# Performance work log

Hardware: AMD Instinct MI355X
Metric: run time of the kernel (lower is better)

Reference implementation:

```python
import jax, jax.numpy as jnp
import numpy as np

NEG_SLOPE = 0.2  # PyG GATConv default negative_slope


def _gat_conv(x, edge_index, W, att_src, att_dst, bias, heads, out_ch, concat):
    """PyG-style GATConv with add_self_loops=False, shared src/dst lin.
    x: [N, F_in], edge_index: [2, E] (row 0 = src j, row 1 = dst i).
    W: [F_in, heads*out_ch]; att_src/att_dst: [heads, out_ch]; bias: [heads*out_ch] or [out_ch].
    """
    N = x.shape[0]
    src, dst = edge_index[0], edge_index[1]
    h = (x @ W).reshape(N, heads, out_ch)                      # [N, H, C]
    a_src = jnp.einsum('nhc,hc->nh', h, att_src)               # [N, H]
    a_dst = jnp.einsum('nhc,hc->nh', h, att_dst)               # [N, H]
    e = a_src[src] + a_dst[dst]                                # [E, H]
    e = jnp.where(e > 0, e, NEG_SLOPE * e)                     # leaky_relu
    # segment softmax over edges sharing the same destination
    m = jax.ops.segment_max(e, dst, num_segments=N)            # [N, H]
    e = jnp.exp(e - m[dst])                                    # [E, H]
    s = jax.ops.segment_sum(e, dst, num_segments=N)            # [N, H]
    alpha = e / (s[dst] + 1e-16)                               # [E, H]
    msg = h[src] * alpha[:, :, None]                           # [E, H, C]
    out = jax.ops.segment_sum(msg, dst, num_segments=N)        # [N, H, C]
    if concat:
        out = out.reshape(N, heads * out_ch)
    else:
        out = out.mean(axis=1)
    return out + bias


def setup_inputs() -> dict:
    key = jax.random.key(0)
    ks = jax.random.split(key, 12)
    N, E = 100000, 1600000
    dinp, dhid, dout, heads = 128, 32, 128, 4
    x = jax.random.normal(ks[0], (N, dinp), dtype=jnp.float32)
    a = jax.random.randint(ks[1], (2, E), 0, N, dtype=jnp.int64)
    s1 = 1.0 / np.sqrt(dinp)
    s2 = 1.0 / np.sqrt(dhid * heads)
    return {
        'x': x,
        'a': a,
        'W1': jax.random.normal(ks[2], (dinp, heads * dhid), dtype=jnp.float32) * s1,
        'att_src1': jax.random.normal(ks[3], (heads, dhid), dtype=jnp.float32) * s1,
        'att_dst1': jax.random.normal(ks[4], (heads, dhid), dtype=jnp.float32) * s1,
        'b1': jnp.zeros((heads * dhid,), dtype=jnp.float32),
        'W2': jax.random.normal(ks[5], (heads * dhid, dout), dtype=jnp.float32) * s2,
        'att_src2': jax.random.normal(ks[6], (1, dout), dtype=jnp.float32) * s2,
        'att_dst2': jax.random.normal(ks[7], (1, dout), dtype=jnp.float32) * s2,
        'b2': jnp.zeros((dout,), dtype=jnp.float32),
    }


def reference(x, a, W1, att_src1, att_dst1, b1, W2, att_src2, att_dst2, b2):
    heads, dhid, dout = 4, 32, 128
    h = _gat_conv(x, a, W1, att_src1, att_dst1, b1, heads, dhid, concat=True)
    h = jax.nn.elu(h)
    out = _gat_conv(h, a, W2, att_src2, att_dst2, b2, 1, dout, concat=False)
    return jax.nn.elu(out)
```

## Files before the change

kernel.cpp:

```cpp
#include <hip/hip_runtime.h>
#include <hip/hip_fp16.h>
#include <math.h>


typedef _Float16 f16x8 __attribute__((ext_vector_type(8)));
typedef float    f32x4 __attribute__((ext_vector_type(4)));


__global__ __launch_bounds__(256) void k_hist(const int* __restrict__ dst,
                                              int* __restrict__ bcnt, int E, int NBUCK) {
    __shared__ int lh[1024];
    int t = threadIdx.x;
    for (int i = t; i < NBUCK; i += 256) lh[i] = 0;
    __syncthreads();
    for (int e = blockIdx.x * 256 + t; e < E; e += gridDim.x * 256)
        atomicAdd(&lh[dst[e] >> 7], 1);
    __syncthreads();
    for (int i = t; i < NBUCK; i += 256) {
        int c = lh[i];
        if (c) atomicAdd(&bcnt[i], c);
    }
}

__global__ void k_bscan(const int* __restrict__ bcnt, int* __restrict__ bbase,
                        int* __restrict__ bcur, int* __restrict__ off,
                        int NBUCK, int N, int E) {
    __shared__ int sd[1024];
    int t = threadIdx.x;
    int v = (t < NBUCK) ? bcnt[t] : 0;
    sd[t] = v; __syncthreads();
    for (int ofs = 1; ofs < 1024; ofs <<= 1) {
        int w = (t >= ofs) ? sd[t - ofs] : 0;
        __syncthreads();
        sd[t] += w;
        __syncthreads();
    }
    if (t < NBUCK) { int ex = sd[t] - v; bbase[t] = ex; bcur[t] = ex; }
    if (t == 0) { bbase[NBUCK] = E; off[N] = E; }
}

__global__ __launch_bounds__(256) void k_binscatter(
    const int* __restrict__ src, const int* __restrict__ dst,
    int* __restrict__ bcur, int* __restrict__ tmp, int E, int NBUCK) {
    __shared__ int lh[1024], lbase[1024];
    int t = threadIdx.x;
    for (int i = t; i < NBUCK; i += 256) lh[i] = 0;
    __syncthreads();
    int tbeg = blockIdx.x * 8192;
    int tend = tbeg + 8192; if (tend > E) tend = E;
    for (int e = tbeg + t; e < tend; e += 256) atomicAdd(&lh[dst[e] >> 7], 1);
    __syncthreads();
    for (int i = t; i < NBUCK; i += 256) {
        int c = lh[i];
        lbase[i] = c ? atomicAdd(&bcur[i], c) : 0;
        lh[i] = 0;
    }
    __syncthreads();
    for (int e = tbeg + t; e < tend; e += 256) {
        int d = dst[e];
        int b = d >> 7;
        int r = atomicAdd(&lh[b], 1);
        tmp[lbase[b] + r] = (src[e] << 7) | (d & 127);
    }
}

__global__ __launch_bounds__(256) void k_bsort(
    const int* __restrict__ tmp, const int* __restrict__ bbase,
    int* __restrict__ off, int* __restrict__ esrc, int N) {
    __shared__ int h[128], hs[128], cur[128];
    int b = blockIdx.x, t = threadIdx.x;
    int base = bbase[b];
    int cnt  = bbase[b + 1] - base;
    int node0 = b << 7;
    if (t < 128) h[t] = 0;
    __syncthreads();
    for (int i = t; i < cnt; i += 256) atomicAdd(&h[tmp[base + i] & 127], 1);
    __syncthreads();
    if (t < 128) hs[t] = h[t];
    __syncthreads();
    for (int ofs = 1; ofs < 128; ofs <<= 1) {
        int w = (t < 128 && t >= ofs) ? hs[t - ofs] : 0;
        __syncthreads();
        if (t < 128) hs[t] += w;
        __syncthreads();
    }
    if (t < 128) {
        int ex = hs[t] - h[t];
        if (node0 + t < N) off[node0 + t] = base + ex;
        cur[t] = base + ex;
    }
    __syncthreads();
    for (int i = t; i < cnt; i += 256) {
        int p = tmp[base + i];
        int pos = atomicAdd(&cur[p & 127], 1);
        esrc[pos] = p >> 7;
    }
}


template <int H, typename TI>
__global__ __launch_bounds__(256, 3) void k_gemm_mfma(
    const TI* __restrict__ X, const float* __restrict__ Wg,
    const float* __restrict__ att_s, const float* __restrict__ att_d,
    __half* __restrict__ Y, float* __restrict__ as_, float* __restrict__ ad_, int N)
{
    __shared__ _Float16 Wf[8][4][512];
    __shared__ _Float16 Xh[64][136];
    const int t = threadIdx.x;
    const int lane = t & 63;
    const int wv = t >> 6;
    const int m = lane & 15;
    const int q = lane >> 4;

    for (int f = t; f < 2048; f += 256) {
        int nt = f >> 8, ks = (f >> 6) & 3, ls = f & 63;
        int qq = ls >> 4, mm = ls & 15;
        int col = nt * 16 + mm;
        int k0  = ks * 32 + qq * 8;
        f16x8 frag;
#pragma unroll
        for (int j = 0; j < 8; j++)
            frag[j] = (_Float16)Wg[(size_t)(k0 + j) * 128 + col];
        *(f16x8*)&Wf[nt][ks][ls * 8] = frag;
    }

    float atts_v[8], attd_v[8];
#pragma unroll
    for (int nt = 0; nt < 8; nt++) {
        atts_v[nt] = att_s[nt * 16 + m];
        attd_v[nt] = att_d[nt * 16 + m];
    }
    __syncthreads();

    for (int base = blockIdx.x * 64; base < N; base += gridDim.x * 64) {
        for (int i = t; i < 1024; i += 256) {
            int r = i >> 4, c8 = i & 15;
            int gr = base + r;
            _Float16* d = &Xh[r][c8 * 8];
            if (gr < N) {
                if constexpr (sizeof(TI) == 4) {
                    const float4* s = (const float4*)((const float*)X + (size_t)gr * 128 + c8 * 8);
                    float4 x0 = s[0], x1 = s[1];
                    d[0] = (_Float16)x0.x; d[1] = (_Float16)x0.y;
                    d[2] = (_Float16)x0.z; d[3] = (_Float16)x0.w;
                    d[4] = (_Float16)x1.x; d[5] = (_Float16)x1.y;
                    d[6] = (_Float16)x1.z; d[7] = (_Float16)x1.w;
                } else {
                    *(uint4*)d = *(const uint4*)((const __half*)X + (size_t)gr * 128 + c8 * 8);
                }
            } else {
                uint4 z; z.x = 0; z.y = 0; z.z = 0; z.w = 0;
                *(uint4*)d = z;
            }
        }
        __syncthreads();

        const int rowb = base + wv * 16;

        f16x8 af[4];
#pragma unroll
        for (int ks = 0; ks < 4; ks++)
            af[ks] = *(const f16x8*)&Xh[wv * 16 + m][ks * 32 + q * 8];

        f32x4 acc[8];
#pragma unroll
        for (int nt = 0; nt < 8; nt++) { acc[nt][0] = 0.f; acc[nt][1] = 0.f; acc[nt][2] = 0.f; acc[nt][3] = 0.f; }

#pragma unroll
        for (int nt = 0; nt < 8; nt++) {
            f16x8 b0v = *(const f16x8*)&Wf[nt][0][lane * 8];
            f16x8 b1v = *(const f16x8*)&Wf[nt][1][lane * 8];
            f16x8 b2v = *(const f16x8*)&Wf[nt][2][lane * 8];
            f16x8 b3v = *(const f16x8*)&Wf[nt][3][lane * 8];
            acc[nt] = __builtin_amdgcn_mfma_f32_16x16x32_f16(af[0], b0v, acc[nt], 0, 0, 0);
            acc[nt] = __builtin_amdgcn_mfma_f32_16x16x32_f16(af[1], b1v, acc[nt], 0, 0, 0);
            acc[nt] = __builtin_amdgcn_mfma_f32_16x16x32_f16(af[2], b2v, acc[nt], 0, 0, 0);
            acc[nt] = __builtin_amdgcn_mfma_f32_16x16x32_f16(af[3], b3v, acc[nt], 0, 0, 0);
        }

#pragma unroll
        for (int nt = 0; nt < 8; nt++) {
#pragma unroll
            for (int i = 0; i < 4; i++) {
                int r = rowb + q * 4 + i;
                if (r < N) Y[(size_t)r * 128 + nt * 16 + m] = __float2half(acc[nt][i]);
            }
        }

        if (H == 4) {
            float ph[4][4], pdv[4][4];
#pragma unroll
            for (int h = 0; h < 4; h++)
#pragma unroll
                for (int i = 0; i < 4; i++) {
                    ph[h][i]  = acc[2 * h][i] * atts_v[2 * h] + acc[2 * h + 1][i] * atts_v[2 * h + 1];
                    pdv[h][i] = acc[2 * h][i] * attd_v[2 * h] + acc[2 * h + 1][i] * attd_v[2 * h + 1];
                }
#pragma unroll
            for (int lvl = 0; lvl < 4; lvl++) {
                const int msk = 1 << lvl;
#pragma unroll
                for (int h = 0; h < 4; h++)
#pragma unroll
                    for (int i = 0; i < 4; i++) {
                        ph[h][i]  += __shfl_xor(ph[h][i], msk, 64);
                        pdv[h][i] += __shfl_xor(pdv[h][i], msk, 64);
                    }
            }
            if (m == 0) {
#pragma unroll
                for (int i = 0; i < 4; i++) {
                    int r = rowb + q * 4 + i;
                    if (r < N) {
#pragma unroll
                        for (int h = 0; h < 4; h++) {
                            as_[(size_t)r * 4 + h] = ph[h][i];
                            ad_[(size_t)r * 4 + h] = pdv[h][i];
                        }
                    }
                }
            }
        } else {
            float ps[4], pdv[4];
#pragma unroll
            for (int i = 0; i < 4; i++) {
                float s = 0.f, dsum = 0.f;
#pragma unroll
                for (int nt = 0; nt < 8; nt++) {
                    s    += acc[nt][i] * atts_v[nt];
                    dsum += acc[nt][i] * attd_v[nt];
                }
                ps[i] = s; pdv[i] = dsum;
            }
#pragma unroll
            for (int lvl = 0; lvl < 4; lvl++) {
                const int msk = 1 << lvl;
#pragma unroll
                for (int i = 0; i < 4; i++) {
                    ps[i]  += __shfl_xor(ps[i], msk, 64);
                    pdv[i] += __shfl_xor(pdv[i], msk, 64);
                }
            }
            if (m == 0) {
#pragma unroll
                for (int i = 0; i < 4; i++) {
                    int r = rowb + q * 4 + i;
                    if (r < N) { as_[r] = ps[i]; ad_[r] = pdv[i]; }
                }
            }
        }
        __syncthreads();
    }
}


template <int H, typename TO>
__global__ __launch_bounds__(256) void k_agg(
    const __half* __restrict__ feat,
    const float* __restrict__ asrc,
    const float* __restrict__ adst,
    const int*   __restrict__ off,
    const int*   __restrict__ esrc,
    const float* __restrict__ bias,
    TO*          __restrict__ out,
    int N)
{
    __shared__ __attribute__((aligned(16))) int   sj[4][64];
    __shared__ __attribute__((aligned(16))) float sp[4][64 * H];

    int wave = threadIdx.x >> 6;
    int lane = threadIdx.x & 63;
    int node = (blockIdx.x * 256 + threadIdx.x) >> 6;
    if (node >= N) return;
    int beg = off[node], end = off[node + 1];

    float adst_i[H];
#pragma unroll
    for (int h = 0; h < H; h++) adst_i[h] = adst[(size_t)node * H + h];

    const int g    = lane >> 4;
    const int sub  = lane & 15;
    const int head = (H == 4) ? (sub >> 2) : 0;
    const __half* fb = feat + sub * 8;

    float o0 = 0.f, o1 = 0.f, o2 = 0.f, o3 = 0.f;
    float o4 = 0.f, o5 = 0.f, o6 = 0.f, o7 = 0.f;
    float ssum = 0.f;

    auto accum8 = [&](const __half* hp, float aa) {
        ssum += aa;
        o0 = fmaf(aa, __half2float(hp[0]), o0);
        o1 = fmaf(aa, __half2float(hp[1]), o1);
        o2 = fmaf(aa, __half2float(hp[2]), o2);
        o3 = fmaf(aa, __half2float(hp[3]), o3);
        o4 = fmaf(aa, __half2float(hp[4]), o4);
        o5 = fmaf(aa, __half2float(hp[5]), o5);
        o6 = fmaf(aa, __half2float(hp[6]), o6);
        o7 = fmaf(aa, __half2float(hp[7]), o7);
    };

    for (int cbeg = beg; cbeg < end; cbeg += 64) {
        int cnt = end - cbeg; if (cnt > 64) cnt = 64;
        if (lane < cnt) {
            int j = esrc[cbeg + lane];
            sj[wave][lane] = j;
            if (H == 4) {
                float4 av = *(const float4*)(asrc + (size_t)j * 4);
                float e;
                e = av.x + adst_i[0]; e = e > 0.f ? e : 0.2f * e; sp[wave][0 * 64 + lane] = __expf(e);
                e = av.y + adst_i[1]; e = e > 0.f ? e : 0.2f * e; sp[wave][1 * 64 + lane] = __expf(e);
                e = av.z + adst_i[2]; e = e > 0.f ? e : 0.2f * e; sp[wave][2 * 64 + lane] = __expf(e);
                e = av.w + adst_i[3]; e = e > 0.f ? e : 0.2f * e; sp[wave][3 * 64 + lane] = __expf(e);
            } else {
                float e = asrc[j] + adst_i[0];
                e = e > 0.f ? e : 0.2f * e;
                sp[wave][lane] = __expf(e);
            }
        }
        asm volatile("s_waitcnt lgkmcnt(0)" ::: "memory");

        for (int b0 = 0; b0 < cnt; b0 += 16) {
            float aa[4]; uint4 hv[4];
#pragma unroll
            for (int u = 0; u < 4; u++) {
                int e  = b0 + 4 * u + g;
                bool ok = e < cnt;
                int ec = ok ? e : 0;
                int j  = sj[wave][ec];
                aa[u]  = ok ? sp[wave][head * 64 + ec] : 0.f;
                hv[u]  = *(const uint4*)(fb + (size_t)j * 128);
            }
            accum8((const __half*)&hv[0], aa[0]);
            accum8((const __half*)&hv[1], aa[1]);
            accum8((const __half*)&hv[2], aa[2]);
            accum8((const __half*)&hv[3], aa[3]);
        }
    }

    o0 += __shfl_xor(o0, 16, 64); o0 += __shfl_xor(o0, 32, 64);
    o1 += __shfl_xor(o1, 16, 64); o1 += __shfl_xor(o1, 32, 64);
    o2 += __shfl_xor(o2, 16, 64); o2 += __shfl_xor(o2, 32, 64);
    o3 += __shfl_xor(o3, 16, 64); o3 += __shfl_xor(o3, 32, 64);
    o4 += __shfl_xor(o4, 16, 64); o4 += __shfl_xor(o4, 32, 64);
    o5 += __shfl_xor(o5, 16, 64); o5 += __shfl_xor(o5, 32, 64);
    o6 += __shfl_xor(o6, 16, 64); o6 += __shfl_xor(o6, 32, 64);
    o7 += __shfl_xor(o7, 16, 64); o7 += __shfl_xor(o7, 32, 64);
    ssum += __shfl_xor(ssum, 16, 64);
    ssum += __shfl_xor(ssum, 32, 64);

    float so0 = o0, so1 = o1;
    so0 = (g == 1) ? o2 : so0;  so1 = (g == 1) ? o3 : so1;
    so0 = (g == 2) ? o4 : so0;  so1 = (g == 2) ? o5 : so1;
    so0 = (g == 3) ? o6 : so0;  so1 = (g == 3) ? o7 : so1;

    const int c2 = sub * 8 + 2 * g;
    float inv = 1.f / (ssum + 1e-16f);
    float r0 = so0 * inv + bias[c2];
    float r1 = so1 * inv + bias[c2 + 1];
    float e0 = __expf(r0) - 1.0f;
    float e1 = __expf(r1) - 1.0f;
    r0 = r0 > 0.f ? r0 : e0;
    r1 = r1 > 0.f ? r1 : e1;

    if constexpr (sizeof(TO) == 2) {
        *(__half2*)((__half*)out + (size_t)node * 128 + c2) = __floats2half2_rn(r0, r1);
    } else {
        *(float2*)((float*)out + (size_t)node * 128 + c2) = make_float2(r0, r1);
    }
}


extern "C" void kernel_launch(void* const* d_in, const int* in_sizes, int n_in,
                              void* d_out, int out_size, void* d_ws, size_t ws_size,
                              hipStream_t stream)
{
    const float* x    = (const float*)d_in[0];
    const int*   a    = (const int*)  d_in[1];
    const float* W1   = (const float*)d_in[2];
    const float* as1w = (const float*)d_in[3];
    const float* ad1w = (const float*)d_in[4];
    const float* b1   = (const float*)d_in[5];
    const float* W2   = (const float*)d_in[6];
    const float* as2w = (const float*)d_in[7];
    const float* ad2w = (const float*)d_in[8];
    const float* b2   = (const float*)d_in[9];

    const int N = in_sizes[0] / 128;
    const int E = in_sizes[1] / 2;
    const int* srcA = a;
    const int* dstA = a + E;
    const int NBUCK = (N + 127) >> 7;

    char* ws = (char*)d_ws;
    size_t o = 0;
    auto alloc = [&](size_t bytes) -> void* {
        void* p = ws + o;
        o += (bytes + 255) & ~(size_t)255;
        return p;
    };
    __half* hbuf  = (__half*)alloc((size_t)N * 128 * 2);
    __half* hact  = (__half*)alloc((size_t)N * 128 * 2);
    float*  as1   = (float*) alloc((size_t)N * 4 * 4);
    float*  ad1   = (float*) alloc((size_t)N * 4 * 4);
    float*  as2   = (float*) alloc((size_t)N * 4);
    float*  ad2   = (float*) alloc((size_t)N * 4);
    int*    off   = (int*)   alloc((size_t)(N + 1) * 4);
    int*    esrc  = (int*)   alloc((size_t)E * 4);
    int*    tmp   = (int*)   alloc((size_t)E * 4);
    int*    bcnt  = (int*)   alloc(1024 * 4);
    int*    bbase = (int*)   alloc(1025 * 4);
    int*    bcur  = (int*)   alloc(1024 * 4);

    hipMemsetAsync(bcnt, 0, (size_t)NBUCK * 4, stream);
    k_hist<<<256, 256, 0, stream>>>(dstA, bcnt, E, NBUCK);
    k_bscan<<<1, 1024, 0, stream>>>(bcnt, bbase, bcur, off, NBUCK, N, E);
    k_binscatter<<<(E + 8191) / 8192, 256, 0, stream>>>(srcA, dstA, bcur, tmp, E, NBUCK);
    k_bsort<<<NBUCK, 256, 0, stream>>>(tmp, bbase, off, esrc, N);

    k_gemm_mfma<4, float><<<768, 256, 0, stream>>>(x, W1, as1w, ad1w, hbuf, as1, ad1, N);
    k_agg<4, __half><<<(N + 3) / 4, 256, 0, stream>>>(hbuf, as1, ad1, off, esrc, b1, hact, N);

    k_gemm_mfma<1, __half><<<768, 256, 0, stream>>>(hact, W2, as2w, ad2w, hbuf, as2, ad2, N);
    k_agg<1, float><<<(N + 3) / 4, 256, 0, stream>>>(hbuf, as2, ad2, off, esrc, b2, (float*)d_out, N);
}
```

Baseline: 340.6 us.

## Fuse layer-1 aggregation with layer-2 GEMM and attention logits

New measurement: 350.3 us. 2.9% more time.

```diff
diff --git a/kernel.cpp b/kernel.cpp
--- a/kernel.cpp
+++ b/kernel.cpp
@@ -24,9 +24,18 @@
 
 __global__ void k_bscan(const int* __restrict__ bcnt, int* __restrict__ bbase,
                         int* __restrict__ bcur, int* __restrict__ off,
-                        int NBUCK, int N, int E) {
+                        int NBUCK, int N, int E,
+                        const float* __restrict__ W2g, _Float16* __restrict__ W2f) {
     __shared__ int sd[1024];
     int t = threadIdx.x;
+    for (int f = t; f < 2048; f += 1024) {
+        int nt = f >> 8, ks = (f >> 6) & 3, ls = f & 63;
+        int col = nt * 16 + (ls & 15);
+        int k0  = ks * 32 + (ls >> 4) * 8;
+#pragma unroll
+        for (int j = 0; j < 8; j++)
+            W2f[(size_t)f * 8 + j] = (_Float16)W2g[(size_t)(k0 + j) * 128 + col];
+    }
     int v = (t < NBUCK) ? bcnt[t] : 0;
     sd[t] = v; __syncthreads();
     for (int ofs = 1; ofs < 1024; ofs <<= 1) {
@@ -254,6 +263,188 @@
 }
 
 
+__global__ __launch_bounds__(256) void k_agg_g2(
+    const __half* __restrict__ feat,
+    const float* __restrict__ asrc,
+    const float* __restrict__ adst,
+    const int*   __restrict__ off,
+    const int*   __restrict__ esrc,
+    const float* __restrict__ bias,
+    const _Float16* __restrict__ W2f,
+    const float* __restrict__ att_s2,
+    const float* __restrict__ att_d2,
+    __half* __restrict__ Y2,
+    float* __restrict__ as2, float* __restrict__ ad2, int N)
+{
+    __shared__ __attribute__((aligned(16))) int      sj[4][64];
+    __shared__ __attribute__((aligned(16))) float    sp[4][256];
+    __shared__ __attribute__((aligned(16))) _Float16 rows[16][136];
+    __shared__ float sps[4][16], spd[4][16];
+
+    const int wave = threadIdx.x >> 6;
+    const int lane = threadIdx.x & 63;
+    const int g    = lane >> 4;
+    const int sub  = lane & 15;
+    const int head = sub >> 2;
+    const __half* fb = feat + sub * 8;
+    const int nodeBase = blockIdx.x * 16;
+
+    for (int it = 0; it < 4; it++) {
+        const int node = nodeBase + wave * 4 + it;
+        int beg = 0, end = 0;
+        float ad0 = 0.f, ad1v = 0.f, ad2v = 0.f, ad3v = 0.f;
+        if (node < N) {
+            beg = off[node]; end = off[node + 1];
+            const float* ap = adst + (size_t)node * 4;
+            ad0 = ap[0]; ad1v = ap[1]; ad2v = ap[2]; ad3v = ap[3];
+        }
+
+        float o0 = 0.f, o1 = 0.f, o2 = 0.f, o3 = 0.f;
+        float o4 = 0.f, o5 = 0.f, o6 = 0.f, o7 = 0.f;
+        float ssum = 0.f;
+
+        auto accum8 = [&](const __half* hp, float aa) {
+            ssum += aa;
+            o0 = fmaf(aa, __half2float(hp[0]), o0);
+            o1 = fmaf(aa, __half2float(hp[1]), o1);
+            o2 = fmaf(aa, __half2float(hp[2]), o2);
+            o3 = fmaf(aa, __half2float(hp[3]), o3);
+            o4 = fmaf(aa, __half2float(hp[4]), o4);
+            o5 = fmaf(aa, __half2float(hp[5]), o5);
+            o6 = fmaf(aa, __half2float(hp[6]), o6);
+            o7 = fmaf(aa, __half2float(hp[7]), o7);
+        };
+
+        for (int cbeg = beg; cbeg < end; cbeg += 64) {
+            int cnt = end - cbeg; if (cnt > 64) cnt = 64;
+            if (lane < cnt) {
+                int j = esrc[cbeg + lane];
+                sj[wave][lane] = j;
+                float4 av = *(const float4*)(asrc + (size_t)j * 4);
+                float e;
+                e = av.x + ad0;  e = e > 0.f ? e : 0.2f * e; sp[wave][0 * 64 + lane] = __expf(e);
+                e = av.y + ad1v; e = e > 0.f ? e : 0.2f * e; sp[wave][1 * 64 + lane] = __expf(e);
+                e = av.z + ad2v; e = e > 0.f ? e : 0.2f * e; sp[wave][2 * 64 + lane] = __expf(e);
+                e = av.w + ad3v; e = e > 0.f ? e : 0.2f * e; sp[wave][3 * 64 + lane] = __expf(e);
+            }
+            asm volatile("s_waitcnt lgkmcnt(0)" ::: "memory");
+
+            for (int b0 = 0; b0 < cnt; b0 += 16) {
+                float aa[4]; uint4 hv[4];
+#pragma unroll
+                for (int u = 0; u < 4; u++) {
+                    int e  = b0 + 4 * u + g;
+                    bool ok = e < cnt;
+                    int ec = ok ? e : 0;
+                    int j  = sj[wave][ec];
+                    aa[u]  = ok ? sp[wave][head * 64 + ec] : 0.f;
+                    hv[u]  = *(const uint4*)(fb + (size_t)j * 128);
+                }
+                accum8((const __half*)&hv[0], aa[0]);
+                accum8((const __half*)&hv[1], aa[1]);
+                accum8((const __half*)&hv[2], aa[2]);
+                accum8((const __half*)&hv[3], aa[3]);
+            }
+        }
+
+        o0 += __shfl_xor(o0, 16, 64); o0 += __shfl_xor(o0, 32, 64);
+        o1 += __shfl_xor(o1, 16, 64); o1 += __shfl_xor(o1, 32, 64);
+        o2 += __shfl_xor(o2, 16, 64); o2 += __shfl_xor(o2, 32, 64);
+        o3 += __shfl_xor(o3, 16, 64); o3 += __shfl_xor(o3, 32, 64);
+        o4 += __shfl_xor(o4, 16, 64); o4 += __shfl_xor(o4, 32, 64);
+        o5 += __shfl_xor(o5, 16, 64); o5 += __shfl_xor(o5, 32, 64);
+        o6 += __shfl_xor(o6, 16, 64); o6 += __shfl_xor(o6, 32, 64);
+        o7 += __shfl_xor(o7, 16, 64); o7 += __shfl_xor(o7, 32, 64);
+        ssum += __shfl_xor(ssum, 16, 64);
+        ssum += __shfl_xor(ssum, 32, 64);
+
+        float so0 = o0, so1 = o1;
+        so0 = (g == 1) ? o2 : so0;  so1 = (g == 1) ? o3 : so1;
+        so0 = (g == 2) ? o4 : so0;  so1 = (g == 2) ? o5 : so1;
+        so0 = (g == 3) ? o6 : so0;  so1 = (g == 3) ? o7 : so1;
+
+        const int c2 = sub * 8 + 2 * g;
+        float inv = 1.f / (ssum + 1e-16f);
+        float r0 = so0 * inv + bias[c2];
+        float r1 = so1 * inv + bias[c2 + 1];
+        float e0 = __expf(r0) - 1.0f;
+        float e1 = __expf(r1) - 1.0f;
+        r0 = r0 > 0.f ? r0 : e0;
+        r1 = r1 > 0.f ? r1 : e1;
+
+        _Float16* rp = &rows[wave * 4 + it][c2];
+        rp[0] = (_Float16)r0;
+        rp[1] = (_Float16)r1;
+    }
+    __syncthreads();
+
+    const int m = lane & 15;
+    const int q = lane >> 4;
+
+    f16x8 af[4];
+#pragma unroll
+    for (int ks = 0; ks < 4; ks++)
+        af[ks] = *(const f16x8*)&rows[m][ks * 32 + q * 8];
+
+    f32x4 acc[2];
+    float a2s[2], a2d[2];
+#pragma unroll
+    for (int u = 0; u < 2; u++) {
+        const int nt = wave * 2 + u;
+        a2s[u] = att_s2[nt * 16 + m];
+        a2d[u] = att_d2[nt * 16 + m];
+        acc[u][0] = 0.f; acc[u][1] = 0.f; acc[u][2] = 0.f; acc[u][3] = 0.f;
+#pragma unroll
+        for (int ks = 0; ks < 4; ks++) {
+            f16x8 bv = *(const f16x8*)(W2f + ((size_t)(nt * 4 + ks) * 512 + lane * 8));
+            acc[u] = __builtin_amdgcn_mfma_f32_16x16x32_f16(af[ks], bv, acc[u], 0, 0, 0);
+        }
+    }
+
+#pragma unroll
+    for (int u = 0; u < 2; u++) {
+        const int col = (wave * 2 + u) * 16 + m;
+#pragma unroll
+        for (int i = 0; i < 4; i++) {
+            int r = nodeBase + q * 4 + i;
+            if (r < N) Y2[(size_t)r * 128 + col] = __float2half(acc[u][i]);
+        }
+    }
+
+    float ps[4], pd[4];
+#pragma unroll
+    for (int i = 0; i < 4; i++) {
+        ps[i] = acc[0][i] * a2s[0] + acc[1][i] * a2s[1];
+        pd[i] = acc[0][i] * a2d[0] + acc[1][i] * a2d[1];
+    }
+#pragma unroll
+    for (int lvl = 0; lvl < 4; lvl++) {
+        const int msk = 1 << lvl;
+#pragma unroll
+        for (int i = 0; i < 4; i++) {
+            ps[i] += __shfl_xor(ps[i], msk, 64);
+            pd[i] += __shfl_xor(pd[i], msk, 64);
+        }
+    }
+    if (m == 0) {
+#pragma unroll
+        for (int i = 0; i < 4; i++) {
+            sps[wave][q * 4 + i] = ps[i];
+            spd[wave][q * 4 + i] = pd[i];
+        }
+    }
+    __syncthreads();
+
+    if (wave == 0 && lane < 16) {
+        int node = nodeBase + lane;
+        if (node < N) {
+            as2[node] = sps[0][lane] + sps[1][lane] + sps[2][lane] + sps[3][lane];
+            ad2[node] = spd[0][lane] + spd[1][lane] + spd[2][lane] + spd[3][lane];
+        }
+    }
+}
+
+
 template <int H, typename TO>
 __global__ __launch_bounds__(256) void k_agg(
     const __half* __restrict__ feat,
@@ -398,28 +589,30 @@
         o += (bytes + 255) & ~(size_t)255;
         return p;
     };
-    __half* hbuf  = (__half*)alloc((size_t)N * 128 * 2);
-    __half* hact  = (__half*)alloc((size_t)N * 128 * 2);
-    float*  as1   = (float*) alloc((size_t)N * 4 * 4);
-    float*  ad1   = (float*) alloc((size_t)N * 4 * 4);
-    float*  as2   = (float*) alloc((size_t)N * 4);
-    float*  ad2   = (float*) alloc((size_t)N * 4);
-    int*    off   = (int*)   alloc((size_t)(N + 1) * 4);
-    int*    esrc  = (int*)   alloc((size_t)E * 4);
-    int*    tmp   = (int*)   alloc((size_t)E * 4);
-    int*    bcnt  = (int*)   alloc(1024 * 4);
-    int*    bbase = (int*)   alloc(1025 * 4);
-    int*    bcur  = (int*)   alloc(1024 * 4);
+    __half*    hbuf = (__half*)   alloc((size_t)N * 128 * 2);
+    __half*    y2   = (__half*)   alloc((size_t)N * 128 * 2);
+    float*     as1  = (float*)    alloc((size_t)N * 4 * 4);
+    float*     ad1  = (float*)    alloc((size_t)N * 4 * 4);
+    float*     as2  = (float*)    alloc((size_t)N * 4);
+    float*     ad2  = (float*)    alloc((size_t)N * 4);
+    int*       off  = (int*)      alloc((size_t)(N + 1) * 4);
+    int*       esrc = (int*)      alloc((size_t)E * 4);
+    int*       tmp  = (int*)      alloc((size_t)E * 4);
+    int*       bcnt = (int*)      alloc(1024 * 4);
+    int*       bbase= (int*)      alloc(1025 * 4);
+    int*       bcur = (int*)      alloc(1024 * 4);
+    _Float16*  w2f  = (_Float16*) alloc((size_t)2048 * 16);
 
     hipMemsetAsync(bcnt, 0, (size_t)NBUCK * 4, stream);
     k_hist<<<256, 256, 0, stream>>>(dstA, bcnt, E, NBUCK);
-    k_bscan<<<1, 1024, 0, stream>>>(bcnt, bbase, bcur, off, NBUCK, N, E);
+    k_bscan<<<1, 1024, 0, stream>>>(bcnt, bbase, bcur, off, NBUCK, N, E, W2, w2f);
     k_binscatter<<<(E + 8191) / 8192, 256, 0, stream>>>(srcA, dstA, bcur, tmp, E, NBUCK);
     k_bsort<<<NBUCK, 256, 0, stream>>>(tmp, bbase, off, esrc, N);
 
     k_gemm_mfma<4, float><<<768, 256, 0, stream>>>(x, W1, as1w, ad1w, hbuf, as1, ad1, N);
-    k_agg<4, __half><<<(N + 3) / 4, 256, 0, stream>>>(hbuf, as1, ad1, off, esrc, b1, hact, N);
-
-    k_gemm_mfma<1, __half><<<768, 256, 0, stream>>>(hact, W2, as2w, ad2w, hbuf, as2, ad2, N);
-    k_agg<1, float><<<(N + 3) / 4, 256, 0, stream>>>(hbuf, as2, ad2, off, esrc, b2, (float*)d_out, N);
-}
+
+    k_agg_g2<<<(N + 15) / 16, 256, 0, stream>>>(hbuf, as1, ad1, off, esrc, b1,
+                                                w2f, as2w, ad2w, y2, as2, ad2, N);
+
+    k_agg<1, float><<<(N + 3) / 4, 256, 0, stream>>>(y2, as2, ad2, off, esrc, b2, (float*)d_out, N);
+}
```

## Replace two-level bucket sort CSR build with global atomic counting sort

Applied to the files above, without the earlier changes.

Result: slower. 495.6 us (+45.5%).

```diff
diff --git a/kernel.cpp b/kernel.cpp
--- a/kernel.cpp
+++ b/kernel.cpp
@@ -7,27 +7,30 @@
 typedef float    f32x4 __attribute__((ext_vector_type(4)));
 
 
-__global__ __launch_bounds__(256) void k_hist(const int* __restrict__ dst,
-                                              int* __restrict__ bcnt, int E, int NBUCK) {
-    __shared__ int lh[1024];
-    int t = threadIdx.x;
-    for (int i = t; i < NBUCK; i += 256) lh[i] = 0;
-    __syncthreads();
-    for (int e = blockIdx.x * 256 + t; e < E; e += gridDim.x * 256)
-        atomicAdd(&lh[dst[e] >> 7], 1);
-    __syncthreads();
-    for (int i = t; i < NBUCK; i += 256) {
-        int c = lh[i];
-        if (c) atomicAdd(&bcnt[i], c);
-    }
-}
-
-__global__ void k_bscan(const int* __restrict__ bcnt, int* __restrict__ bbase,
-                        int* __restrict__ bcur, int* __restrict__ off,
-                        int NBUCK, int N, int E) {
+__global__ __launch_bounds__(256) void k_count(const int* __restrict__ dst,
+                                               int* __restrict__ cnt, int E) {
+    for (int e = blockIdx.x * 256 + threadIdx.x; e < E; e += gridDim.x * 256)
+        atomicAdd(&cnt[dst[e]], 1);
+}
+
+__global__ void k_ssum(const int* __restrict__ cnt, int* __restrict__ bsum, int N) {
     __shared__ int sd[1024];
     int t = threadIdx.x;
-    int v = (t < NBUCK) ? bcnt[t] : 0;
+    int i = blockIdx.x * 1024 + t;
+    sd[t] = (i < N) ? cnt[i] : 0;
+    __syncthreads();
+    for (int ofs = 512; ofs > 0; ofs >>= 1) {
+        if (t < ofs) sd[t] += sd[t + ofs];
+        __syncthreads();
+    }
+    if (t == 0) bsum[blockIdx.x] = sd[0];
+}
+
+__global__ void k_stop(const int* __restrict__ bsum, int* __restrict__ bbase,
+                       int nb, int N, int E, int* __restrict__ off) {
+    __shared__ int sd[1024];
+    int t = threadIdx.x;
+    int v = (t < nb) ? bsum[t] : 0;
     sd[t] = v; __syncthreads();
     for (int ofs = 1; ofs < 1024; ofs <<= 1) {
         int w = (t >= ofs) ? sd[t - ofs] : 0;
@@ -35,65 +38,36 @@
         sd[t] += w;
         __syncthreads();
     }
-    if (t < NBUCK) { int ex = sd[t] - v; bbase[t] = ex; bcur[t] = ex; }
-    if (t == 0) { bbase[NBUCK] = E; off[N] = E; }
-}
-
-__global__ __launch_bounds__(256) void k_binscatter(
+    if (t < nb) bbase[t] = sd[t] - v;
+    if (t == 0) off[N] = E;
+}
+
+__global__ void k_sfin(const int* __restrict__ cnt, const int* __restrict__ bbase,
+                       int* __restrict__ off, int* __restrict__ cur, int N) {
+    __shared__ int sd[1024];
+    int t = threadIdx.x;
+    int i = blockIdx.x * 1024 + t;
+    int v = (i < N) ? cnt[i] : 0;
+    sd[t] = v; __syncthreads();
+    for (int ofs = 1; ofs < 1024; ofs <<= 1) {
+        int w = (t >= ofs) ? sd[t - ofs] : 0;
+        __syncthreads();
+        sd[t] += w;
+        __syncthreads();
+    }
+    if (i < N) {
+        int ex = bbase[blockIdx.x] + sd[t] - v;
+        off[i] = ex;
+        cur[i] = ex;
+    }
+}
+
+__global__ __launch_bounds__(256) void k_scatter(
     const int* __restrict__ src, const int* __restrict__ dst,
-    int* __restrict__ bcur, int* __restrict__ tmp, int E, int NBUCK) {
-    __shared__ int lh[1024], lbase[1024];
-    int t = threadIdx.x;
-    for (int i = t; i < NBUCK; i += 256) lh[i] = 0;
-    __syncthreads();
-    int tbeg = blockIdx.x * 8192;
-    int tend = tbeg + 8192; if (tend > E) tend = E;
-    for (int e = tbeg + t; e < tend; e += 256) atomicAdd(&lh[dst[e] >> 7], 1);
-    __syncthreads();
-    for (int i = t; i < NBUCK; i += 256) {
-        int c = lh[i];
-        lbase[i] = c ? atomicAdd(&bcur[i], c) : 0;
-        lh[i] = 0;
-    }
-    __syncthreads();
-    for (int e = tbeg + t; e < tend; e += 256) {
-        int d = dst[e];
-        int b = d >> 7;
-        int r = atomicAdd(&lh[b], 1);
-        tmp[lbase[b] + r] = (src[e] << 7) | (d & 127);
-    }
-}
-
-__global__ __launch_bounds__(256) void k_bsort(
-    const int* __restrict__ tmp, const int* __restrict__ bbase,
-    int* __restrict__ off, int* __restrict__ esrc, int N) {
-    __shared__ int h[128], hs[128], cur[128];
-    int b = blockIdx.x, t = threadIdx.x;
-    int base = bbase[b];
-    int cnt  = bbase[b + 1] - base;
-    int node0 = b << 7;
-    if (t < 128) h[t] = 0;
-    __syncthreads();
-    for (int i = t; i < cnt; i += 256) atomicAdd(&h[tmp[base + i] & 127], 1);
-    __syncthreads();
-    if (t < 128) hs[t] = h[t];
-    __syncthreads();
-    for (int ofs = 1; ofs < 128; ofs <<= 1) {
-        int w = (t < 128 && t >= ofs) ? hs[t - ofs] : 0;
-        __syncthreads();
-        if (t < 128) hs[t] += w;
-        __syncthreads();
-    }
-    if (t < 128) {
-        int ex = hs[t] - h[t];
-        if (node0 + t < N) off[node0 + t] = base + ex;
-        cur[t] = base + ex;
-    }
-    __syncthreads();
-    for (int i = t; i < cnt; i += 256) {
-        int p = tmp[base + i];
-        int pos = atomicAdd(&cur[p & 127], 1);
-        esrc[pos] = p >> 7;
+    int* __restrict__ cur, int* __restrict__ esrc, int E) {
+    for (int e = blockIdx.x * 256 + threadIdx.x; e < E; e += gridDim.x * 256) {
+        int p = atomicAdd(&cur[dst[e]], 1);
+        esrc[p] = src[e];
     }
 }
 
@@ -389,7 +363,6 @@
     const int E = in_sizes[1] / 2;
     const int* srcA = a;
     const int* dstA = a + E;
-    const int NBUCK = (N + 127) >> 7;
 
     char* ws = (char*)d_ws;
     size_t o = 0;
@@ -406,16 +379,19 @@
     float*  ad2   = (float*) alloc((size_t)N * 4);
     int*    off   = (int*)   alloc((size_t)(N + 1) * 4);
     int*    esrc  = (int*)   alloc((size_t)E * 4);
-    int*    tmp   = (int*)   alloc((size_t)E * 4);
-    int*    bcnt  = (int*)   alloc(1024 * 4);
-    int*    bbase = (int*)   alloc(1025 * 4);
-    int*    bcur  = (int*)   alloc(1024 * 4);
-
-    hipMemsetAsync(bcnt, 0, (size_t)NBUCK * 4, stream);
-    k_hist<<<256, 256, 0, stream>>>(dstA, bcnt, E, NBUCK);
-    k_bscan<<<1, 1024, 0, stream>>>(bcnt, bbase, bcur, off, NBUCK, N, E);
-    k_binscatter<<<(E + 8191) / 8192, 256, 0, stream>>>(srcA, dstA, bcur, tmp, E, NBUCK);
-    k_bsort<<<NBUCK, 256, 0, stream>>>(tmp, bbase, off, esrc, N);
+    int*    cnt   = (int*)   alloc((size_t)N * 4);
+    int*    cur   = (int*)   alloc((size_t)N * 4);
+    int*    bsum  = (int*)   alloc(1024 * 4);
+    int*    bbase = (int*)   alloc(1024 * 4);
+
+    const int nb = (N + 1023) >> 10;
+
+    hipMemsetAsync(cnt, 0, (size_t)N * 4, stream);
+    k_count<<<256, 256, 0, stream>>>(dstA, cnt, E);
+    k_ssum<<<nb, 1024, 0, stream>>>(cnt, bsum, N);
+    k_stop<<<1, 1024, 0, stream>>>(bsum, bbase, nb, N, E, off);
+    k_sfin<<<nb, 1024, 0, stream>>>(cnt, bbase, off, cur, N);
+    k_scatter<<<512, 256, 0, stream>>>(srcA, dstA, cur, esrc, E);
 
     k_gemm_mfma<4, float><<<768, 256, 0, stream>>>(x, W1, as1w, ad1w, hbuf, as1, ad1, N);
     k_agg<4, __half><<<(N + 3) / 4, 256, 0, stream>>>(hbuf, as1, ad1, off, esrc, b1, hact, N);
```
